# Kernel tuning notes

Measured on AMD Instinct MI355X. Metric: run time of the kernel, lower is better.

The kernel has to match this reference:

```python
import jax, jax.numpy as jnp
import numpy as np

B, W, H, I, L = 64, 4096, 128, 128, 2


def setup_inputs() -> dict:
    key = jax.random.key(0)
    ks = jax.random.split(key, 16)
    f = lambda k, s: jax.random.normal(k, s, dtype=jnp.float32) * 0.05
    return dict(
        input=f(ks[0], (B, 1, I)),
        h0=f(ks[1], (L, B, H)),
        c0=f(ks[2], (L, B, H)),
        encoder_output=f(ks[3], (B, W, H)),
        att_W=f(ks[4], (1, 2 * H)), att_b=f(ks[5], (1,)),
        inp_W=f(ks[6], (I, H + I)), inp_b=f(ks[7], (I,)),
        W_ih0=f(ks[8], (4 * H, I)), W_hh0=f(ks[9], (4 * H, H)),
        b_ih0=f(ks[10], (4 * H,)), b_hh0=f(ks[11], (4 * H,)),
        W_ih1=f(ks[12], (4 * H, H)), W_hh1=f(ks[13], (4 * H, H)),
        b_ih1=f(ks[14], (4 * H,)), b_hh1=f(ks[15], (4 * H,)),
    )


def _lstm_cell(x, h, c, W_ih, W_hh, b_ih, b_hh):
    # PyTorch gate order: i, f, g, o
    gates = x @ W_ih.T + h @ W_hh.T + b_ih + b_hh
    i, f, g, o = jnp.split(gates, 4, axis=-1)
    c_new = jax.nn.sigmoid(f) * c + jax.nn.sigmoid(i) * jnp.tanh(g)
    h_new = jax.nn.sigmoid(o) * jnp.tanh(c_new)
    return h_new, c_new


def reference(input, h0, c0, encoder_output, att_W, att_b, inp_W, inp_b,
              W_ih0, W_hh0, b_ih0, b_hh0, W_ih1, W_hh1, b_ih1, b_hh1):
    att_state = h0[-1] * c0[-1]                       # (B, H)
    # att_line over concat(enc_word, att_state): split the (1, 2H) weight.
    wa_enc, wa_st = att_W[0, :H], att_W[0, H:]
    scores = encoder_output @ wa_enc + (att_state @ wa_st + att_b[0])[:, None]  # (B, W)
    # Faithful to original: a leading zeros column is prepended, then
    # softmax is taken over [:, 0:-1] -> keeps the zero column, drops the
    # LAST word's score.
    zero_col = jnp.zeros((scores.shape[0], 1), scores.dtype)
    full = jnp.concatenate([zero_col, scores], axis=1)  # (B, W+1)
    weight = jax.nn.softmax(full[:, :-1], axis=1)        # (B, W)
    x = jnp.einsum('bw,bwh->bh', weight, encoder_output)  # (B, H)
    xin = jnp.concatenate([x, input[:, 0, :]], axis=1) @ inp_W.T + inp_b  # (B, I)
    # 2-layer LSTM, single time step (eval mode -> inter-layer dropout off)
    h1, c1 = _lstm_cell(xin, h0[0], c0[0], W_ih0, W_hh0, b_ih0, b_hh0)
    h2, c2 = _lstm_cell(h1, h0[1], c0[1], W_ih1, W_hh1, b_ih1, b_hh1)
    output = h2[:, None, :]                              # (B, 1, H)
    return output, jnp.stack([h1, h2]), jnp.stack([c1, c2])
```

## Files before the change

### kernel.cpp

```cpp
#include <hip/hip_runtime.h>

#define BB 64
#define WW 4096
#define HH 128
#define NCHUNK 32
#define CROWS 128
#define PSTRIDE 132

__device__ inline float sigmoidf(float x) { return 1.0f / (1.0f + expf(-x)); }

__global__ void fused_attention(const float* __restrict__ enc,
                                const float* __restrict__ h0,
                                const float* __restrict__ c0,
                                const float* __restrict__ attW,
                                const float* __restrict__ attb,
                                float* __restrict__ partials) {
    __shared__ float s_wa[128];
    __shared__ float s_red[128];
    __shared__ float s_sc[CROWS];
    __shared__ float s_p[CROWS];
    __shared__ float racc[16 * 128];
    __shared__ float s_bias, s_m, s_extra;

    const int t = threadIdx.x;
    const int b = blockIdx.x >> 5;
    const int chunk = blockIdx.x & 31;
    const int w0 = chunk * CROWS;

    if (t < 128) {
        s_wa[t] = attW[t];
        float hv = h0[BB * HH + b * HH + t];
        float cv = c0[BB * HH + b * HH + t];
        s_red[t] = hv * cv * attW[HH + t];
    }
    __syncthreads();
    for (int s = 64; s > 0; s >>= 1) {
        if (t < s) s_red[t] += s_red[t + s];
        __syncthreads();
    }
    if (t == 0) s_bias = s_red[0] + attb[0];
    __syncthreads();
    const float bias = s_bias;

    const int seg = t & 15;
    const int rg  = t >> 4;
    float wseg[8];
#pragma unroll
    for (int j = 0; j < 8; j++) wseg[j] = s_wa[seg * 8 + j];

    float4 ra[8], rc[8];
#pragma unroll
    for (int pass = 0; pass < 8; pass++) {
        const int r = pass * 16 + rg;
        const float4* p = (const float4*)(enc + ((size_t)b * WW + w0 + r) * HH + seg * 8);
        ra[pass] = p[0];
        rc[pass] = p[1];
        float d = ra[pass].x * wseg[0] + ra[pass].y * wseg[1]
                + ra[pass].z * wseg[2] + ra[pass].w * wseg[3]
                + rc[pass].x * wseg[4] + rc[pass].y * wseg[5]
                + rc[pass].z * wseg[6] + rc[pass].w * wseg[7];
        d += __shfl_xor(d, 8, 16);
        d += __shfl_xor(d, 4, 16);
        d += __shfl_xor(d, 2, 16);
        d += __shfl_xor(d, 1, 16);
        if (seg == 0) s_sc[r] = d + bias;
    }

    if (chunk > 0 && t < 16) {
        const float4* p = (const float4*)(enc + ((size_t)b * WW + w0 - 1) * HH + t * 8);
        float4 a = p[0], c = p[1];
        float d = a.x * wseg[0] + a.y * wseg[1] + a.z * wseg[2] + a.w * wseg[3]
                + c.x * wseg[4] + c.y * wseg[5] + c.z * wseg[6] + c.w * wseg[7];
        d += __shfl_xor(d, 8, 16);
        d += __shfl_xor(d, 4, 16);
        d += __shfl_xor(d, 2, 16);
        d += __shfl_xor(d, 1, 16);
        if (t == 0) s_extra = d + bias;
    }
    __syncthreads();

    if (t < 128) {
        float v;
        if (t == 0) v = (chunk > 0) ? s_extra : -1e30f;
        else        v = s_sc[t - 1];
        s_p[t] = v;
    }
    __syncthreads();

    if (t < 64) s_red[t] = fmaxf(s_p[t], s_p[t + 64]);
    __syncthreads();
    for (int s = 32; s > 0; s >>= 1) {
        if (t < s) s_red[t] = fmaxf(s_red[t], s_red[t + s]);
        __syncthreads();
    }
    if (t == 0) s_m = s_red[0];
    __syncthreads();
    const float m = s_m;

    if (t < 128) s_p[t] = expf(s_p[t] - m);
    __syncthreads();
    if (t < 64) s_red[t] = s_p[t] + s_p[t + 64];
    __syncthreads();
    for (int s = 32; s > 0; s >>= 1) {
        if (t < s) s_red[t] += s_red[t + s];
        __syncthreads();
    }

    float acc8[8];
#pragma unroll
    for (int j = 0; j < 8; j++) acc8[j] = 0.f;
#pragma unroll
    for (int pass = 0; pass < 8; pass++) {
        const int r = pass * 16 + rg;
        const float pw = s_p[r];
        acc8[0] += pw * ra[pass].x; acc8[1] += pw * ra[pass].y;
        acc8[2] += pw * ra[pass].z; acc8[3] += pw * ra[pass].w;
        acc8[4] += pw * rc[pass].x; acc8[5] += pw * rc[pass].y;
        acc8[6] += pw * rc[pass].z; acc8[7] += pw * rc[pass].w;
    }
#pragma unroll
    for (int j = 0; j < 8; j++) racc[rg * 128 + seg * 8 + j] = acc8[j];
    __syncthreads();

    float* out = partials + (size_t)(b * NCHUNK + chunk) * PSTRIDE;
    if (t < 128) {
        float s = 0.f;
#pragma unroll
        for (int w2 = 0; w2 < 16; w2++) s += racc[w2 * 128 + t];
        out[t] = s;
    }
    if (t == 128) out[128] = m;
    if (t == 129) out[129] = s_red[0];
}

__global__ void tail_kernel(const float* __restrict__ partials,
                            const float* __restrict__ enc,
                            const float* __restrict__ input,
                            const float* __restrict__ inpW,
                            const float* __restrict__ inpb,
                            const float* __restrict__ Wih0,
                            const float* __restrict__ Whh0,
                            const float* __restrict__ bih0,
                            const float* __restrict__ bhh0,
                            const float* __restrict__ Wih1,
                            const float* __restrict__ Whh1,
                            const float* __restrict__ bih1,
                            const float* __restrict__ bhh1,
                            const float* __restrict__ h0,
                            const float* __restrict__ c0,
                            float* __restrict__ out) {
    __shared__ float lm[NCHUNK], llv[NCHUNK], ls[NCHUNK];
    __shared__ float sM, sL;
    __shared__ float xc[256];
    __shared__ float sxv[128];
    __shared__ float shv[128];
    __shared__ float sh1[128];
    __shared__ float shv2[128];
    __shared__ float gates[512];

    const int b = blockIdx.x;
    const int t = threadIdx.x;

    if (t < NCHUNK) {
        const float* pp = partials + (size_t)(b * NCHUNK + t) * PSTRIDE;
        lm[t] = pp[128];
        llv[t] = pp[129];
    }
    __syncthreads();
    if (t == 0) {
        float M = 0.0f;
        for (int c = 0; c < NCHUNK; c++) M = fmaxf(M, lm[c]);
        float L = expf(-M);
        for (int c = 0; c < NCHUNK; c++) {
            float s = expf(lm[c] - M);
            ls[c] = s;
            L += s * llv[c];
        }
        sM = M; sL = L;
    }
    __syncthreads();

    if (t < 128) {
        float xv = expf(-sM) * enc[(size_t)b * WW * HH + t];
        for (int c = 0; c < NCHUNK; c++)
            xv += ls[c] * partials[(size_t)(b * NCHUNK + c) * PSTRIDE + t];
        xc[t] = xv / sL;
        xc[128 + t] = input[b * HH + t];
    }
    __syncthreads();

    if (t < 128) {
        float a = inpb[t];
        const float4* wr = (const float4*)(inpW + (size_t)t * 256);
#pragma unroll
        for (int k = 0; k < 64; k++) {
            float4 w4 = wr[k];
            a += xc[4 * k] * w4.x + xc[4 * k + 1] * w4.y
               + xc[4 * k + 2] * w4.z + xc[4 * k + 3] * w4.w;
        }
        sxv[t] = a;
        shv[t] = h0[b * HH + t];
        shv2[t] = h0[BB * HH + b * HH + t];
    }
    __syncthreads();

    {
        float g = bih0[t] + bhh0[t];
        const float4* wi = (const float4*)(Wih0 + (size_t)t * 128);
        const float4* wh = (const float4*)(Whh0 + (size_t)t * 128);
#pragma unroll
        for (int k = 0; k < 32; k++) {
            float4 a = wi[k], c = wh[k];
            g += sxv[4 * k] * a.x + sxv[4 * k + 1] * a.y + sxv[4 * k + 2] * a.z + sxv[4 * k + 3] * a.w
               + shv[4 * k] * c.x + shv[4 * k + 1] * c.y + shv[4 * k + 2] * c.z + shv[4 * k + 3] * c.w;
        }
        gates[t] = g;
    }
    __syncthreads();
    if (t < 128) {
        float ig = sigmoidf(gates[t]);
        float fg = sigmoidf(gates[128 + t]);
        float gg = tanhf(gates[256 + t]);
        float og = sigmoidf(gates[384 + t]);
        float cn = fg * c0[b * HH + t] + ig * gg;
        float hn = og * tanhf(cn);
        out[8192 + b * HH + t] = hn;
        out[24576 + b * HH + t] = cn;
        sh1[t] = hn;
    }
    __syncthreads();

    {
        float g = bih1[t] + bhh1[t];
        const float4* wi = (const float4*)(Wih1 + (size_t)t * 128);
        const float4* wh = (const float4*)(Whh1 + (size_t)t * 128);
#pragma unroll
        for (int k = 0; k < 32; k++) {
            float4 a = wi[k], c = wh[k];
            g += sh1[4 * k] * a.x + sh1[4 * k + 1] * a.y + sh1[4 * k + 2] * a.z + sh1[4 * k + 3] * a.w
               + shv2[4 * k] * c.x + shv2[4 * k + 1] * c.y + shv2[4 * k + 2] * c.z + shv2[4 * k + 3] * c.w;
        }
        gates[t] = g;
    }
    __syncthreads();
    if (t < 128) {
        float ig = sigmoidf(gates[t]);
        float fg = sigmoidf(gates[128 + t]);
        float gg = tanhf(gates[256 + t]);
        float og = sigmoidf(gates[384 + t]);
        float cn = fg * c0[BB * HH + b * HH + t] + ig * gg;
        float hn = og * tanhf(cn);
        out[b * HH + t] = hn;
        out[16384 + b * HH + t] = hn;
        out[32768 + b * HH + t] = cn;
    }
}

extern "C" void kernel_launch(void* const* d_in, const int* in_sizes, int n_in,
                              void* d_out, int out_size, void* d_ws, size_t ws_size,
                              hipStream_t stream) {
    const float* input = (const float*)d_in[0];
    const float* h0    = (const float*)d_in[1];
    const float* c0    = (const float*)d_in[2];
    const float* enc   = (const float*)d_in[3];
    const float* attW  = (const float*)d_in[4];
    const float* attb  = (const float*)d_in[5];
    const float* inpW  = (const float*)d_in[6];
    const float* inpb  = (const float*)d_in[7];
    const float* Wih0  = (const float*)d_in[8];
    const float* Whh0  = (const float*)d_in[9];
    const float* bih0  = (const float*)d_in[10];
    const float* bhh0  = (const float*)d_in[11];
    const float* Wih1  = (const float*)d_in[12];
    const float* Whh1  = (const float*)d_in[13];
    const float* bih1  = (const float*)d_in[14];
    const float* bhh1  = (const float*)d_in[15];

    float* partials = (float*)d_ws;

    fused_attention<<<BB * NCHUNK, 256, 0, stream>>>(enc, h0, c0, attW, attb, partials);
    tail_kernel<<<BB, 512, 0, stream>>>(partials, enc, input, inpW, inpb,
                                        Wih0, Whh0, bih0, bhh0,
                                        Wih1, Whh1, bih1, bhh1,
                                        h0, c0, (float*)d_out);
}
```

Baseline: 272.9 us.

## Fuse attention and LSTM tail into one kernel via last-block atomic counter

Merges the attention-partials kernel and the LSTM tail kernel into a single launch. Each block writes its partials, fences, and bumps a per-batch atomic counter; the last block to arrive for a batch runs the softmax merge, input projection and both LSTM cells, with 256 threads each covering two gate rows. This is meant to remove the second kernel launch and the gap between kernels, at the cost of a memset launch, serialised tail work on the winning blocks, and extra LDS per block that may lower occupancy.

```diff
diff --git a/kernel.cpp b/kernel.cpp
--- a/kernel.cpp
+++ b/kernel.cpp
@@ -9,18 +9,33 @@
 
 __device__ inline float sigmoidf(float x) { return 1.0f / (1.0f + expf(-x)); }
 
-__global__ void fused_attention(const float* __restrict__ enc,
-                                const float* __restrict__ h0,
-                                const float* __restrict__ c0,
-                                const float* __restrict__ attW,
-                                const float* __restrict__ attb,
-                                float* __restrict__ partials) {
+__global__ __launch_bounds__(256, 4)
+void fused_all(const float* __restrict__ enc,
+               const float* __restrict__ h0,
+               const float* __restrict__ c0,
+               const float* __restrict__ attW,
+               const float* __restrict__ attb,
+               const float* __restrict__ input,
+               const float* __restrict__ inpW,
+               const float* __restrict__ inpb,
+               const float* __restrict__ Wih0,
+               const float* __restrict__ Whh0,
+               const float* __restrict__ bih0,
+               const float* __restrict__ bhh0,
+               const float* __restrict__ Wih1,
+               const float* __restrict__ Whh1,
+               const float* __restrict__ bih1,
+               const float* __restrict__ bhh1,
+               float* __restrict__ partials,
+               int* __restrict__ counters,
+               float* __restrict__ out) {
     __shared__ float s_wa[128];
     __shared__ float s_red[128];
     __shared__ float s_sc[CROWS];
     __shared__ float s_p[CROWS];
     __shared__ float racc[16 * 128];
     __shared__ float s_bias, s_m, s_extra;
+    __shared__ int s_win;
 
     const int t = threadIdx.x;
     const int b = blockIdx.x >> 5;
@@ -122,33 +137,26 @@
     for (int j = 0; j < 8; j++) racc[rg * 128 + seg * 8 + j] = acc8[j];
     __syncthreads();
 
-    float* out = partials + (size_t)(b * NCHUNK + chunk) * PSTRIDE;
+    float* pout = partials + (size_t)(b * NCHUNK + chunk) * PSTRIDE;
     if (t < 128) {
         float s = 0.f;
 #pragma unroll
         for (int w2 = 0; w2 < 16; w2++) s += racc[w2 * 128 + t];
-        out[t] = s;
-    }
-    if (t == 128) out[128] = m;
-    if (t == 129) out[129] = s_red[0];
-}
-
-__global__ void tail_kernel(const float* __restrict__ partials,
-                            const float* __restrict__ enc,
-                            const float* __restrict__ input,
-                            const float* __restrict__ inpW,
-                            const float* __restrict__ inpb,
-                            const float* __restrict__ Wih0,
-                            const float* __restrict__ Whh0,
-                            const float* __restrict__ bih0,
-                            const float* __restrict__ bhh0,
-                            const float* __restrict__ Wih1,
-                            const float* __restrict__ Whh1,
-                            const float* __restrict__ bih1,
-                            const float* __restrict__ bhh1,
-                            const float* __restrict__ h0,
-                            const float* __restrict__ c0,
-                            float* __restrict__ out) {
+        pout[t] = s;
+    }
+    if (t == 128) pout[128] = m;
+    if (t == 129) pout[129] = s_red[0];
+
+    __threadfence();
+    __syncthreads();
+    if (t == 0) {
+        int old = atomicAdd(&counters[b], 1);
+        s_win = (old == NCHUNK - 1) ? 1 : 0;
+    }
+    __syncthreads();
+    if (!s_win) return;
+    __threadfence();
+
     __shared__ float lm[NCHUNK], llv[NCHUNK], ls[NCHUNK];
     __shared__ float sM, sL;
     __shared__ float xc[256];
@@ -158,9 +166,6 @@
     __shared__ float shv2[128];
     __shared__ float gates[512];
 
-    const int b = blockIdx.x;
-    const int t = threadIdx.x;
-
     if (t < NCHUNK) {
         const float* pp = partials + (size_t)(b * NCHUNK + t) * PSTRIDE;
         lm[t] = pp[128];
@@ -204,17 +209,19 @@
     }
     __syncthreads();
 
-    {
-        float g = bih0[t] + bhh0[t];
-        const float4* wi = (const float4*)(Wih0 + (size_t)t * 128);
-        const float4* wh = (const float4*)(Whh0 + (size_t)t * 128);
+#pragma unroll
+    for (int rr = 0; rr < 2; rr++) {
+        const int row = t + rr * 256;
+        float g = bih0[row] + bhh0[row];
+        const float4* wi = (const float4*)(Wih0 + (size_t)row * 128);
+        const float4* wh = (const float4*)(Whh0 + (size_t)row * 128);
 #pragma unroll
         for (int k = 0; k < 32; k++) {
             float4 a = wi[k], c = wh[k];
             g += sxv[4 * k] * a.x + sxv[4 * k + 1] * a.y + sxv[4 * k + 2] * a.z + sxv[4 * k + 3] * a.w
                + shv[4 * k] * c.x + shv[4 * k + 1] * c.y + shv[4 * k + 2] * c.z + shv[4 * k + 3] * c.w;
         }
-        gates[t] = g;
+        gates[row] = g;
     }
     __syncthreads();
     if (t < 128) {
@@ -230,17 +237,19 @@
     }
     __syncthreads();
 
-    {
-        float g = bih1[t] + bhh1[t];
-        const float4* wi = (const float4*)(Wih1 + (size_t)t * 128);
-        const float4* wh = (const float4*)(Whh1 + (size_t)t * 128);
+#pragma unroll
+    for (int rr = 0; rr < 2; rr++) {
+        const int row = t + rr * 256;
+        float g = bih1[row] + bhh1[row];
+        const float4* wi = (const float4*)(Wih1 + (size_t)row * 128);
+        const float4* wh = (const float4*)(Whh1 + (size_t)row * 128);
 #pragma unroll
         for (int k = 0; k < 32; k++) {
             float4 a = wi[k], c = wh[k];
             g += sh1[4 * k] * a.x + sh1[4 * k + 1] * a.y + sh1[4 * k + 2] * a.z + sh1[4 * k + 3] * a.w
                + shv2[4 * k] * c.x + shv2[4 * k + 1] * c.y + shv2[4 * k + 2] * c.z + shv2[4 * k + 3] * c.w;
         }
-        gates[t] = g;
+        gates[row] = g;
     }
     __syncthreads();
     if (t < 128) {
@@ -277,10 +286,12 @@
     const float* bhh1  = (const float*)d_in[15];
 
     float* partials = (float*)d_ws;
-
-    fused_attention<<<BB * NCHUNK, 256, 0, stream>>>(enc, h0, c0, attW, attb, partials);
-    tail_kernel<<<BB, 512, 0, stream>>>(partials, enc, input, inpW, inpb,
-                                        Wih0, Whh0, bih0, bhh0,
-                                        Wih1, Whh1, bih1, bhh1,
-                                        h0, c0, (float*)d_out);
+    int* counters   = (int*)(partials + (size_t)BB * NCHUNK * PSTRIDE);
+
+    hipMemsetAsync(counters, 0, BB * sizeof(int), stream);
+    fused_all<<<BB * NCHUNK, 256, 0, stream>>>(enc, h0, c0, attW, attb,
+                                               input, inpW, inpb,
+                                               Wih0, Whh0, bih0, bhh0,
+                                               Wih1, Whh1, bih1, bhh1,
+                                               partials, counters, (float*)d_out);
 }
```

Result: slower. 644.1 us (+136.1%).
